# Kernel optimization log

Measured on AMD Instinct MI355X. Metric: run time of the kernel, lower is better.

Reference implementation:

```python
import jax, jax.numpy as jnp
import numpy as np

N_NODES = 100000
N_EDGES = 1600000
IN_CH, HID_CH, OUT_CH = 128, 128, 64


def _sage_conv(x, src, dst, Wl, bl, Wr, num_nodes):
    # PyG SAGEConv (aggr='mean', root_weight=True):
    #   out_i = W_l @ mean_{j in N(i)} x_j + b_l + W_r @ x_i
    msgs = x[src]                                            # [E, d] gather
    agg = jax.ops.segment_sum(msgs, dst, num_segments=num_nodes)   # [N, d]
    cnt = jax.ops.segment_sum(jnp.ones((src.shape[0],), x.dtype), dst,
                              num_segments=num_nodes)              # [N]
    mean = agg / jnp.maximum(cnt, 1.0)[:, None]
    return mean @ Wl.T + bl + x @ Wr.T


def setup_inputs() -> dict:
    key = jax.random.key(0)
    ks = jax.random.split(key, 8)
    x = jax.random.normal(ks[0], (N_NODES, IN_CH), dtype=jnp.float32)
    edge_index = jax.random.randint(ks[1], (2, N_EDGES), 0, N_NODES, dtype=jnp.int32)
    s1 = 1.0 / np.sqrt(IN_CH)
    s2 = 1.0 / np.sqrt(HID_CH)
    Wl1 = jax.random.uniform(ks[2], (HID_CH, IN_CH), jnp.float32, -s1, s1)
    bl1 = jax.random.uniform(ks[3], (HID_CH,), jnp.float32, -s1, s1)
    Wr1 = jax.random.uniform(ks[4], (HID_CH, IN_CH), jnp.float32, -s1, s1)
    Wl2 = jax.random.uniform(ks[5], (OUT_CH, HID_CH), jnp.float32, -s2, s2)
    bl2 = jax.random.uniform(ks[6], (OUT_CH,), jnp.float32, -s2, s2)
    Wr2 = jax.random.uniform(ks[7], (OUT_CH, HID_CH), jnp.float32, -s2, s2)
    return {"x": x, "edge_index": edge_index, "Wl1": Wl1, "bl1": bl1,
            "Wr1": Wr1, "Wl2": Wl2, "bl2": bl2, "Wr2": Wr2}


def reference(x, edge_index, Wl1, bl1, Wr1, Wl2, bl2, Wr2):
    src, dst = edge_index[0], edge_index[1]
    n = x.shape[0]
    h = _sage_conv(x, src, dst, Wl1, bl1, Wr1, n)
    h = jax.nn.relu(h)  # dropout is identity in eval mode
    out = _sage_conv(h, src, dst, Wl2, bl2, Wr2, n)
    return out
```

## Files before the change

### kernel.cpp

```cpp
#include <hip/hip_runtime.h>
#include <hip/hip_bf16.h>
#include <stdint.h>

#define IN_CH 128
#define NPB   448
#define NBUCK 224
#define CAP   8192
#define PART_EPB 2048
#define SRC_BITS 17
#define SRC_MASK ((1 << SRC_BITS) - 1)

typedef short v8s __attribute__((ext_vector_type(8)));
typedef float v4f __attribute__((ext_vector_type(4)));
typedef float v2f __attribute__((ext_vector_type(2)));
typedef ushort v4u __attribute__((ext_vector_type(4)));

__device__ __forceinline__ ushort f2b(float f) {
    return ((__hip_bfloat16_raw)__float2bfloat16(f)).x;
}
__device__ __forceinline__ float b2f(ushort u) {
    __hip_bfloat16_raw r; r.x = u;
    return __bfloat162float((__hip_bfloat16)r);
}

#define ACC4(r) {                                                            \
    a01 += (v2f){__uint_as_float((r).x << 16),                               \
                 __uint_as_float((r).x & 0xffff0000u)};                      \
    a23 += (v2f){__uint_as_float((r).y << 16),                               \
                 __uint_as_float((r).y & 0xffff0000u)};                      \
    a45 += (v2f){__uint_as_float((r).z << 16),                               \
                 __uint_as_float((r).z & 0xffff0000u)};                      \
    a67 += (v2f){__uint_as_float((r).w << 16),                               \
                 __uint_as_float((r).w & 0xffff0000u)}; }

__global__ __launch_bounds__(256) void k_part_gemm1(
    const int* __restrict__ src, const int* __restrict__ dst,
    int* __restrict__ cursor, int* __restrict__ ebuf, int E, int PB,
    const float* __restrict__ Af,
    const float* __restrict__ WlF, const float* __restrict__ WrF,
    ushort* __restrict__ qb, ushort* __restrict__ pbb, int N) {
    __shared__ __align__(16) char smem[69632];
    int tid = threadIdx.x;

    if ((int)blockIdx.x < PB) {
        int* sedge = (int*)smem;
        int* sdst  = (int*)(smem + 8192);
        int* h     = (int*)(smem + 16384);
        int* lofs  = h + NBUCK;
        int* gbase = lofs + NBUCK;
        int* lcur  = gbase + NBUCK;
        int* ssc   = lcur + NBUCK;
        unsigned char* sbuck = (unsigned char*)(ssc + 256);

        int eb0 = blockIdx.x * PART_EPB;
        int cnt = min(PART_EPB, E - eb0);

        if (tid < NBUCK) { h[tid] = 0; lcur[tid] = 0; }
        __syncthreads();
        for (int i = tid; i < cnt; i += 256) {
            int d = dst[eb0 + i];
            sdst[i] = d;
            atomicAdd(&h[d / NPB], 1);
        }
        __syncthreads();
        int v = (tid < NBUCK) ? h[tid] : 0;
        ssc[tid] = v;
        __syncthreads();
        for (int off = 1; off < 256; off <<= 1) {
            int val = (tid >= off) ? ssc[tid - off] : 0;
            __syncthreads();
            ssc[tid] += val;
            __syncthreads();
        }
        int excl = ssc[tid] - v;
        if (tid < NBUCK) {
            lofs[tid] = excl;
            gbase[tid] = tid * CAP + atomicAdd(&cursor[tid], v);
        }
        __syncthreads();
        for (int i = tid; i < cnt; i += 256) {
            int s0 = src[eb0 + i];
            int d0 = sdst[i];
            int b = d0 / NPB;
            int dl = d0 - b * NPB;
            int p = atomicAdd(&lcur[b], 1);
            int slot = lofs[b] + p;
            sedge[slot] = (dl << SRC_BITS) | s0;
            sbuck[slot] = (unsigned char)b;
        }
        __syncthreads();
        for (int i = tid; i < cnt; i += 256) {
            int b = sbuck[i];
            int pos = gbase[b] + (i - lofs[b]);
            if (pos < (b + 1) * CAP) ebuf[pos] = sedge[i];
        }
        return;
    }

    const int OC = 256;
    const int NT = OC / 16;
    const int LDW = 128 + 8;
    ushort* Wlds = (ushort*)smem;

    int gb = blockIdx.x - PB;
    if (gb == 0 && tid < 16) {
        v8s z = {0, 0, 0, 0, 0, 0, 0, 0};
        *(v8s*)(qb + (size_t)N * 128 + tid * 8) = z;
    }

    for (int it = 0; it < OC / 16; it++) {
        int idx = it * 256 + tid;
        int r = idx >> 4, kc = (idx & 15) * 8;
        const float* Wrow = (r < OC / 2) ? (WlF + (size_t)r * 128)
                                         : (WrF + (size_t)(r - OC / 2) * 128);
        float4 w0 = *(const float4*)(Wrow + kc);
        float4 w1 = *(const float4*)(Wrow + kc + 4);
        v8s wv;
        wv[0] = (short)f2b(w0.x); wv[1] = (short)f2b(w0.y);
        wv[2] = (short)f2b(w0.z); wv[3] = (short)f2b(w0.w);
        wv[4] = (short)f2b(w1.x); wv[5] = (short)f2b(w1.y);
        wv[6] = (short)f2b(w1.z); wv[7] = (short)f2b(w1.w);
        *(v8s*)((short*)Wlds + r * LDW + kc) = wv;
    }
    __syncthreads();

    int wave = tid >> 6;
    int lane = tid & 63;
    int m16 = lane & 15;
    int quad = lane >> 4;
    int rowbase = gb * 128 + wave * 32;

    v4f acc[2][NT];
#pragma unroll
    for (int mt = 0; mt < 2; mt++)
#pragma unroll
        for (int t = 0; t < NT; t++) acc[mt][t] = {0.f, 0.f, 0.f, 0.f};

    int ar0 = min(rowbase + m16, N - 1);
    int ar1 = min(rowbase + 16 + m16, N - 1);

#pragma unroll
    for (int ks = 0; ks < 4; ks++) {
        int k0 = ks * 32 + quad * 8;
        float4 f00 = *(const float4*)(Af + (size_t)ar0 * 128 + k0);
        float4 f01 = *(const float4*)(Af + (size_t)ar0 * 128 + k0 + 4);
        float4 f10 = *(const float4*)(Af + (size_t)ar1 * 128 + k0);
        float4 f11 = *(const float4*)(Af + (size_t)ar1 * 128 + k0 + 4);
        v8s a0, a1;
        a0[0] = (short)f2b(f00.x); a0[1] = (short)f2b(f00.y);
        a0[2] = (short)f2b(f00.z); a0[3] = (short)f2b(f00.w);
        a0[4] = (short)f2b(f01.x); a0[5] = (short)f2b(f01.y);
        a0[6] = (short)f2b(f01.z); a0[7] = (short)f2b(f01.w);
        a1[0] = (short)f2b(f10.x); a1[1] = (short)f2b(f10.y);
        a1[2] = (short)f2b(f10.z); a1[3] = (short)f2b(f10.w);
        a1[4] = (short)f2b(f11.x); a1[5] = (short)f2b(f11.y);
        a1[6] = (short)f2b(f11.z); a1[7] = (short)f2b(f11.w);
#pragma unroll
        for (int t = 0; t < NT; t++) {
            v8s b = *(const v8s*)((const short*)Wlds + (t * 16 + m16) * LDW + k0);
            acc[0][t] = __builtin_amdgcn_mfma_f32_16x16x32_bf16(a0, b, acc[0][t], 0, 0, 0);
            acc[1][t] = __builtin_amdgcn_mfma_f32_16x16x32_bf16(a1, b, acc[1][t], 0, 0, 0);
        }
    }

#pragma unroll
    for (int mt = 0; mt < 2; mt++) {
        int orow0 = rowbase + mt * 16 + quad * 4;
#pragma unroll
        for (int r = 0; r < 4; r++) {
            int orow = orow0 + r;
            if (orow < N) {
#pragma unroll
                for (int t = 0; t < NT; t++) {
                    int c = t * 16 + m16;
                    float v = acc[mt][t][r];
                    if (c < 128) qb[(size_t)orow * 128 + c] = f2b(v);
                    else pbb[(size_t)orow * 128 + (c - 128)] = f2b(v);
                }
            }
        }
    }
}

__global__ __launch_bounds__(256) void k_bbuild(
    const int* __restrict__ ebuf, const int* __restrict__ cursor,
    int2* __restrict__ rowdeg, int* __restrict__ col, int N) {
    __shared__ int sdeg[NPB];
    __shared__ int scur[NPB];
    __shared__ int ssum[256];
    int b = blockIdx.x, tid = threadIdx.x;
    int base = b * NPB;
    int nodes = min(NPB, N - base);
    int e0 = b * CAP;
    int e1 = e0 + min(cursor[b], CAP);

    for (int i = tid; i < NPB; i += 256) sdeg[i] = 0;
    __syncthreads();
    for (int e = e0 + tid; e < e1; e += 256)
        atomicAdd(&sdeg[((unsigned)ebuf[e]) >> SRC_BITS], 1);
    __syncthreads();
    int d0 = 0, d1 = 0;
    if (tid < 224) { d0 = sdeg[2 * tid]; d1 = sdeg[2 * tid + 1]; }
    int ts = d0 + d1;
    ssum[tid] = ts;
    __syncthreads();
    for (int off = 1; off < 256; off <<= 1) {
        int val = (tid >= off) ? ssum[tid - off] : 0;
        __syncthreads();
        ssum[tid] += val;
        __syncthreads();
    }
    int excl = ssum[tid] - ts;
    if (tid < 224) {
        scur[2 * tid] = excl;
        scur[2 * tid + 1] = excl + d0;
        if (2 * tid < nodes)
            rowdeg[base + 2 * tid] = make_int2(e0 + excl, d0);
        if (2 * tid + 1 < nodes)
            rowdeg[base + 2 * tid + 1] = make_int2(e0 + excl + d0, d1);
    }
    __syncthreads();
    for (int e = e0 + tid; e < e1; e += 256) {
        int w = ebuf[e];
        int dl = ((unsigned)w) >> SRC_BITS;
        int p = atomicAdd(&scur[dl], 1);
        col[e0 + p] = w & SRC_MASK;
    }
}

__global__ __launch_bounds__(256) void k_wgemm2(
    const ushort* __restrict__ Ab,
    const float* __restrict__ WlF, const float* __restrict__ WrF,
    ushort* __restrict__ qb, float* __restrict__ pbf, int N) {
    const int OC = 128;
    const int NT = OC / 16;
    const int LDW = 128 + 8;
    __shared__ ushort Wlds[OC * LDW];

    int tid = threadIdx.x;
    if (blockIdx.x == 0 && tid < 8) {
        v8s z = {0, 0, 0, 0, 0, 0, 0, 0};
        *(v8s*)(qb + (size_t)N * 64 + tid * 8) = z;
    }
    for (int it = 0; it < OC / 16; it++) {
        int idx = it * 256 + tid;
        int r = idx >> 4, kc = (idx & 15) * 8;
        const float* Wrow = (r < OC / 2) ? (WlF + (size_t)r * 128)
                                         : (WrF + (size_t)(r - OC / 2) * 128);
        float4 w0 = *(const float4*)(Wrow + kc);
        float4 w1 = *(const float4*)(Wrow + kc + 4);
        v8s wv;
        wv[0] = (short)f2b(w0.x); wv[1] = (short)f2b(w0.y);
        wv[2] = (short)f2b(w0.z); wv[3] = (short)f2b(w0.w);
        wv[4] = (short)f2b(w1.x); wv[5] = (short)f2b(w1.y);
        wv[6] = (short)f2b(w1.z); wv[7] = (short)f2b(w1.w);
        *(v8s*)((short*)Wlds + r * LDW + kc) = wv;
    }
    __syncthreads();

    int wave = tid >> 6;
    int lane = tid & 63;
    int m16 = lane & 15;
    int quad = lane >> 4;
    int rowbase = blockIdx.x * 128 + wave * 32;

    v4f acc[2][NT];
#pragma unroll
    for (int mt = 0; mt < 2; mt++)
#pragma unroll
        for (int t = 0; t < NT; t++) acc[mt][t] = {0.f, 0.f, 0.f, 0.f};

    int ar0 = min(rowbase + m16, N - 1);
    int ar1 = min(rowbase + 16 + m16, N - 1);

#pragma unroll
    for (int ks = 0; ks < 4; ks++) {
        int k0 = ks * 32 + quad * 8;
        v8s a0 = *(const v8s*)((const short*)Ab + (size_t)ar0 * 128 + k0);
        v8s a1 = *(const v8s*)((const short*)Ab + (size_t)ar1 * 128 + k0);
#pragma unroll
        for (int t = 0; t < NT; t++) {
            v8s b = *(const v8s*)((const short*)Wlds + (t * 16 + m16) * LDW + k0);
            acc[0][t] = __builtin_amdgcn_mfma_f32_16x16x32_bf16(a0, b, acc[0][t], 0, 0, 0);
            acc[1][t] = __builtin_amdgcn_mfma_f32_16x16x32_bf16(a1, b, acc[1][t], 0, 0, 0);
        }
    }

#pragma unroll
    for (int mt = 0; mt < 2; mt++) {
        int orow0 = rowbase + mt * 16 + quad * 4;
#pragma unroll
        for (int r = 0; r < 4; r++) {
            int orow = orow0 + r;
            if (orow < N) {
#pragma unroll
                for (int t = 0; t < NT; t++) {
                    int c = t * 16 + m16;
                    float v = acc[mt][t][r];
                    if (c < 64) qb[(size_t)orow * 64 + c] = f2b(v);
                    else pbf[(size_t)orow * 64 + (c - 64)] = v;
                }
            }
        }
    }
}

__global__ __launch_bounds__(256, 8) void k_agg1(
    const int2* __restrict__ rowdeg,
    const int* __restrict__ col, const ushort* __restrict__ q1b,
    const ushort* __restrict__ p1b, const float* __restrict__ bias,
    ushort* __restrict__ hb, int N) {
    int node = blockIdx.x * (blockDim.x >> 6) + (threadIdx.x >> 6);
    int lane = threadIdx.x & 63;
    if (node >= N) return;
    int2 rd = rowdeg[node];
    int s0 = rd.x, dn = rd.y;
    int s1 = s0 + dn;
    int g = lane >> 4;
    int ch = 8 * (lane & 15);
    v4u pb = *(const v4u*)((const ushort*)p1b + (size_t)node * 128 + ch);
    v4u pb2 = *(const v4u*)((const ushort*)p1b + (size_t)node * 128 + ch + 4);
    int last = (dn > 0) ? (s1 - 1) : s0;
    v2f a01 = {0.f, 0.f}, a23 = {0.f, 0.f}, a45 = {0.f, 0.f}, a67 = {0.f, 0.f};
    int j = s0;
    do {
        int i0 = j + g,      i1 = j + 4 + g,  i2 = j + 8 + g,  i3 = j + 12 + g;
        int i4 = j + 16 + g, i5 = j + 20 + g, i6 = j + 24 + g, i7 = j + 28 + g;
        int t0 = col[min(i0, last)];
        int t1 = col[min(i1, last)];
        int t2 = col[min(i2, last)];
        int t3 = col[min(i3, last)];
        int t4 = col[min(i4, last)];
        int t5 = col[min(i5, last)];
        int t6 = col[min(i6, last)];
        int t7 = col[min(i7, last)];
        int c0 = (i0 < s1) ? t0 : N;
        int c1 = (i1 < s1) ? t1 : N;
        int c2 = (i2 < s1) ? t2 : N;
        int c3 = (i3 < s1) ? t3 : N;
        int c4 = (i4 < s1) ? t4 : N;
        int c5 = (i5 < s1) ? t5 : N;
        int c6 = (i6 < s1) ? t6 : N;
        int c7 = (i7 < s1) ? t7 : N;
        uint4 r0 = *(const uint4*)(q1b + ((uint)c0 * 128u + (uint)ch));
        uint4 r1 = *(const uint4*)(q1b + ((uint)c1 * 128u + (uint)ch));
        uint4 r2 = *(const uint4*)(q1b + ((uint)c2 * 128u + (uint)ch));
        uint4 r3 = *(const uint4*)(q1b + ((uint)c3 * 128u + (uint)ch));
        uint4 r4 = *(const uint4*)(q1b + ((uint)c4 * 128u + (uint)ch));
        uint4 r5 = *(const uint4*)(q1b + ((uint)c5 * 128u + (uint)ch));
        uint4 r6 = *(const uint4*)(q1b + ((uint)c6 * 128u + (uint)ch));
        uint4 r7 = *(const uint4*)(q1b + ((uint)c7 * 128u + (uint)ch));
        ACC4(r0); ACC4(r1); ACC4(r2); ACC4(r3);
        ACC4(r4); ACC4(r5); ACC4(r6); ACC4(r7);
        j += 32;
    } while (j < s1);
    float s[8] = {a01.x, a01.y, a23.x, a23.y, a45.x, a45.y, a67.x, a67.y};
#pragma unroll
    for (int k = 0; k < 8; k++) {
        s[k] += __shfl_xor(s[k], 16);
        s[k] += __shfl_xor(s[k], 32);
    }
    if (g == 0) {
        float inv = (dn > 0) ? 1.0f / (float)dn : 0.0f;
        float4 bi0 = *(const float4*)(bias + ch);
        float4 bi1 = *(const float4*)(bias + ch + 4);
        v8s o;
        o[0] = (short)f2b(fmaxf(s[0] * inv + b2f(pb.x) + bi0.x, 0.f));
        o[1] = (short)f2b(fmaxf(s[1] * inv + b2f(pb.y) + bi0.y, 0.f));
        o[2] = (short)f2b(fmaxf(s[2] * inv + b2f(pb.z) + bi0.z, 0.f));
        o[3] = (short)f2b(fmaxf(s[3] * inv + b2f(pb.w) + bi0.w, 0.f));
        o[4] = (short)f2b(fmaxf(s[4] * inv + b2f(pb2.x) + bi1.x, 0.f));
        o[5] = (short)f2b(fmaxf(s[5] * inv + b2f(pb2.y) + bi1.y, 0.f));
        o[6] = (short)f2b(fmaxf(s[6] * inv + b2f(pb2.z) + bi1.z, 0.f));
        o[7] = (short)f2b(fmaxf(s[7] * inv + b2f(pb2.w) + bi1.w, 0.f));
        *(v8s*)(hb + (size_t)node * 128 + ch) = o;
    }
}

__global__ __launch_bounds__(256, 8) void k_agg2(
    const int2* __restrict__ rowdeg,
    const int* __restrict__ col, const ushort* __restrict__ q2,
    const float* __restrict__ p2, const float* __restrict__ bias,
    float* __restrict__ out, int N) {
    int node = blockIdx.x * (blockDim.x >> 6) + (threadIdx.x >> 6);
    int lane = threadIdx.x & 63;
    if (node >= N) return;
    int2 rd = rowdeg[node];
    int s0 = rd.x, dn = rd.y;
    int s1 = s0 + dn;
    int g = lane >> 3;
    int ch = 8 * (lane & 7);
    v4f p0 = *(const v4f*)(p2 + (size_t)node * 64 + ch);
    v4f p1 = *(const v4f*)(p2 + (size_t)node * 64 + ch + 4);
    int last = (dn > 0) ? (s1 - 1) : s0;
    v2f a01 = {0.f, 0.f}, a23 = {0.f, 0.f}, a45 = {0.f, 0.f}, a67 = {0.f, 0.f};
    int j = s0;
    do {
        int i0 = j + g, i1 = j + 8 + g, i2 = j + 16 + g, i3 = j + 24 + g;
        int t0 = col[min(i0, last)];
        int t1 = col[min(i1, last)];
        int t2 = col[min(i2, last)];
        int t3 = col[min(i3, last)];
        int c0 = (i0 < s1) ? t0 : N;
        int c1 = (i1 < s1) ? t1 : N;
        int c2 = (i2 < s1) ? t2 : N;
        int c3 = (i3 < s1) ? t3 : N;
        uint4 r0 = *(const uint4*)(q2 + ((uint)c0 * 64u + (uint)ch));
        uint4 r1 = *(const uint4*)(q2 + ((uint)c1 * 64u + (uint)ch));
        uint4 r2 = *(const uint4*)(q2 + ((uint)c2 * 64u + (uint)ch));
        uint4 r3 = *(const uint4*)(q2 + ((uint)c3 * 64u + (uint)ch));
        ACC4(r0); ACC4(r1); ACC4(r2); ACC4(r3);
        j += 32;
    } while (j < s1);
    float s[8] = {a01.x, a01.y, a23.x, a23.y, a45.x, a45.y, a67.x, a67.y};
#pragma unroll
    for (int k = 0; k < 8; k++) {
        s[k] += __shfl_xor(s[k], 8);
        s[k] += __shfl_xor(s[k], 16);
        s[k] += __shfl_xor(s[k], 32);
    }
    if (g == 0) {
        float inv = (dn > 0) ? 1.0f / (float)dn : 0.0f;
        float4 bi0 = *(const float4*)(bias + ch);
        float4 bi1 = *(const float4*)(bias + ch + 4);
        v4f o0, o1;
        o0[0] = s[0] * inv + p0[0] + bi0.x;
        o0[1] = s[1] * inv + p0[1] + bi0.y;
        o0[2] = s[2] * inv + p0[2] + bi0.z;
        o0[3] = s[3] * inv + p0[3] + bi0.w;
        o1[0] = s[4] * inv + p1[0] + bi1.x;
        o1[1] = s[5] * inv + p1[1] + bi1.y;
        o1[2] = s[6] * inv + p1[2] + bi1.z;
        o1[3] = s[7] * inv + p1[3] + bi1.w;
        *(v4f*)(out + (size_t)node * 64 + ch) = o0;
        *(v4f*)(out + (size_t)node * 64 + ch + 4) = o1;
    }
}

extern "C" void kernel_launch(void* const* d_in, const int* in_sizes, int n_in,
                              void* d_out, int out_size, void* d_ws, size_t ws_size,
                              hipStream_t stream) {
    const float* x   = (const float*)d_in[0];
    const int* ei    = (const int*)d_in[1];
    const float* Wl1 = (const float*)d_in[2];
    const float* bl1 = (const float*)d_in[3];
    const float* Wr1 = (const float*)d_in[4];
    const float* Wl2 = (const float*)d_in[5];
    const float* bl2 = (const float*)d_in[6];
    const float* Wr2 = (const float*)d_in[7];

    const int N = in_sizes[0] / IN_CH;
    const int E = in_sizes[1] / 2;
    const int* src = ei;
    const int* dst = ei + E;

    char* p = (char*)d_ws;
    auto carve = [&](size_t bytes) -> void* {
        void* q = (void*)p;
        p += (bytes + 255) & ~(size_t)255;
        return q;
    };
    int* cursor   = (int*)carve(NBUCK * 4);
    int* ebuf     = (int*)carve((size_t)NBUCK * CAP * 4);
    int* col      = (int*)carve((size_t)NBUCK * CAP * 4 + 256);
    int2* rowdeg  = (int2*)carve((size_t)N * 8);
    ushort* q1b   = (ushort*)carve(((size_t)N + 1) * 128 * 2);
    ushort* p1b   = (ushort*)carve((size_t)N * 128 * 2);
    ushort* hb    = (ushort*)carve((size_t)N * 128 * 2);
    ushort* q2    = (ushort*)carve(((size_t)N + 1) * 64 * 2);
    float* p2     = (float*)carve((size_t)N * 64 * 4);
    (void)ws_size; (void)n_in;

    float* out = (float*)d_out;
    (void)out_size;

    const int PB  = (E + PART_EPB - 1) / PART_EPB;
    const int GB  = (N + 127) / 128;

    (void)hipMemsetAsync(cursor, 0, NBUCK * 4, stream);
    k_part_gemm1<<<PB + GB, 256, 0, stream>>>(
        src, dst, cursor, ebuf, E, PB, x, Wl1, Wr1, q1b, p1b, N);

    k_bbuild<<<NBUCK, 256, 0, stream>>>(ebuf, cursor, rowdeg, col, N);

    k_agg1<<<(N + 3) / 4, 256, 0, stream>>>(rowdeg, col, q1b, p1b, bl1, hb, N);

    k_wgemm2<<<GB, 256, 0, stream>>>(hb, Wl2, Wr2, q2, p2, N);
    k_agg2<<<(N + 3) / 4, 256, 0, stream>>>(rowdeg, col, q2, p2, bl2, out, N);
}
```

Before: 284.3 us.

## Pair bucket CSR build with layer-1 GEMM instead of edge partitioning

The edge partitioning pass becomes its own small kernel. The per-bucket CSR build is merged with the layer-1 dense GEMM into one launch, so the 224 bbuild blocks run alongside the GEMM blocks rather than as a separate serial launch. Partition blocks no longer carry the GEMM's large shared-memory footprint, and the sbuck array grows from bytes to ints. The risk is that bbuild blocks now hold the GEMM-sized shared memory allocation, which can lower their occupancy.

```diff
diff --git a/kernel.cpp b/kernel.cpp
--- a/kernel.cpp
+++ b/kernel.cpp
@@ -33,76 +33,119 @@
     a67 += (v2f){__uint_as_float((r).w << 16),                               \
                  __uint_as_float((r).w & 0xffff0000u)}; }
 
-__global__ __launch_bounds__(256) void k_part_gemm1(
+__global__ __launch_bounds__(256) void k_part(
     const int* __restrict__ src, const int* __restrict__ dst,
-    int* __restrict__ cursor, int* __restrict__ ebuf, int E, int PB,
+    int* __restrict__ cursor, int* __restrict__ ebuf, int E) {
+    __shared__ int sedge[PART_EPB];
+    __shared__ int sdst[PART_EPB];
+    __shared__ int sbuck[PART_EPB];
+    __shared__ int h[NBUCK], lofs[NBUCK], gbase[NBUCK], lcur[NBUCK];
+    __shared__ int ssc[256];
+
+    int tid = threadIdx.x;
+    int eb0 = blockIdx.x * PART_EPB;
+    int cnt = min(PART_EPB, E - eb0);
+
+    if (tid < NBUCK) { h[tid] = 0; lcur[tid] = 0; }
+    __syncthreads();
+    for (int i = tid; i < cnt; i += 256) {
+        int d = dst[eb0 + i];
+        sdst[i] = d;
+        atomicAdd(&h[d / NPB], 1);
+    }
+    __syncthreads();
+    int v = (tid < NBUCK) ? h[tid] : 0;
+    ssc[tid] = v;
+    __syncthreads();
+    for (int off = 1; off < 256; off <<= 1) {
+        int val = (tid >= off) ? ssc[tid - off] : 0;
+        __syncthreads();
+        ssc[tid] += val;
+        __syncthreads();
+    }
+    int excl = ssc[tid] - v;
+    if (tid < NBUCK) {
+        lofs[tid] = excl;
+        gbase[tid] = tid * CAP + atomicAdd(&cursor[tid], v);
+    }
+    __syncthreads();
+    for (int i = tid; i < cnt; i += 256) {
+        int s0 = src[eb0 + i];
+        int d0 = sdst[i];
+        int b = d0 / NPB;
+        int dl = d0 - b * NPB;
+        int p = atomicAdd(&lcur[b], 1);
+        int slot = lofs[b] + p;
+        sedge[slot] = (dl << SRC_BITS) | s0;
+        sbuck[slot] = b;
+    }
+    __syncthreads();
+    for (int i = tid; i < cnt; i += 256) {
+        int b = sbuck[i];
+        int pos = gbase[b] + (i - lofs[b]);
+        if (pos < (b + 1) * CAP) ebuf[pos] = sedge[i];
+    }
+}
+
+__global__ __launch_bounds__(256) void k_bbuild_gemm1(
+    const int* __restrict__ ebuf, const int* __restrict__ cursor,
+    int2* __restrict__ rowdeg, int* __restrict__ col,
     const float* __restrict__ Af,
     const float* __restrict__ WlF, const float* __restrict__ WrF,
     ushort* __restrict__ qb, ushort* __restrict__ pbb, int N) {
-    __shared__ __align__(16) char smem[69632];
-    int tid = threadIdx.x;
-
-    if ((int)blockIdx.x < PB) {
-        int* sedge = (int*)smem;
-        int* sdst  = (int*)(smem + 8192);
-        int* h     = (int*)(smem + 16384);
-        int* lofs  = h + NBUCK;
-        int* gbase = lofs + NBUCK;
-        int* lcur  = gbase + NBUCK;
-        int* ssc   = lcur + NBUCK;
-        unsigned char* sbuck = (unsigned char*)(ssc + 256);
-
-        int eb0 = blockIdx.x * PART_EPB;
-        int cnt = min(PART_EPB, E - eb0);
-
-        if (tid < NBUCK) { h[tid] = 0; lcur[tid] = 0; }
-        __syncthreads();
-        for (int i = tid; i < cnt; i += 256) {
-            int d = dst[eb0 + i];
-            sdst[i] = d;
-            atomicAdd(&h[d / NPB], 1);
-        }
-        __syncthreads();
-        int v = (tid < NBUCK) ? h[tid] : 0;
-        ssc[tid] = v;
-        __syncthreads();
-        for (int off = 1; off < 256; off <<= 1) {
-            int val = (tid >= off) ? ssc[tid - off] : 0;
-            __syncthreads();
-            ssc[tid] += val;
-            __syncthreads();
-        }
-        int excl = ssc[tid] - v;
-        if (tid < NBUCK) {
-            lofs[tid] = excl;
-            gbase[tid] = tid * CAP + atomicAdd(&cursor[tid], v);
-        }
-        __syncthreads();
-        for (int i = tid; i < cnt; i += 256) {
-            int s0 = src[eb0 + i];
-            int d0 = sdst[i];
-            int b = d0 / NPB;
-            int dl = d0 - b * NPB;
-            int p = atomicAdd(&lcur[b], 1);
-            int slot = lofs[b] + p;
-            sedge[slot] = (dl << SRC_BITS) | s0;
-            sbuck[slot] = (unsigned char)b;
-        }
-        __syncthreads();
-        for (int i = tid; i < cnt; i += 256) {
-            int b = sbuck[i];
-            int pos = gbase[b] + (i - lofs[b]);
-            if (pos < (b + 1) * CAP) ebuf[pos] = sedge[i];
-        }
-        return;
-    }
-
     const int OC = 256;
     const int NT = OC / 16;
     const int LDW = 128 + 8;
-    ushort* Wlds = (ushort*)smem;
-
-    int gb = blockIdx.x - PB;
+    __shared__ ushort Wlds[OC * LDW];
+    __shared__ int sdeg[NPB];
+    __shared__ int scur[NPB];
+    __shared__ int ssum[256];
+
+    int tid = threadIdx.x;
+
+    if (blockIdx.x < NBUCK) {
+        int b = blockIdx.x;
+        int base = b * NPB;
+        int nodes = min(NPB, N - base);
+        int e0 = b * CAP;
+        int e1 = e0 + min(cursor[b], CAP);
+
+        for (int i = tid; i < NPB; i += 256) sdeg[i] = 0;
+        __syncthreads();
+        for (int e = e0 + tid; e < e1; e += 256)
+            atomicAdd(&sdeg[((unsigned)ebuf[e]) >> SRC_BITS], 1);
+        __syncthreads();
+        int d0 = 0, d1 = 0;
+        if (tid < 224) { d0 = sdeg[2 * tid]; d1 = sdeg[2 * tid + 1]; }
+        int ts = d0 + d1;
+        ssum[tid] = ts;
+        __syncthreads();
+        for (int off = 1; off < 256; off <<= 1) {
+            int val = (tid >= off) ? ssum[tid - off] : 0;
+            __syncthreads();
+            ssum[tid] += val;
+            __syncthreads();
+        }
+        int excl = ssum[tid] - ts;
+        if (tid < 224) {
+            scur[2 * tid] = excl;
+            scur[2 * tid + 1] = excl + d0;
+            if (2 * tid < nodes)
+                rowdeg[base + 2 * tid] = make_int2(e0 + excl, d0);
+            if (2 * tid + 1 < nodes)
+                rowdeg[base + 2 * tid + 1] = make_int2(e0 + excl + d0, d1);
+        }
+        __syncthreads();
+        for (int e = e0 + tid; e < e1; e += 256) {
+            int w = ebuf[e];
+            int dl = ((unsigned)w) >> SRC_BITS;
+            int p = atomicAdd(&scur[dl], 1);
+            col[e0 + p] = w & SRC_MASK;
+        }
+        return;
+    }
+
+    int gb = blockIdx.x - NBUCK;
     if (gb == 0 && tid < 16) {
         v8s z = {0, 0, 0, 0, 0, 0, 0, 0};
         *(v8s*)(qb + (size_t)N * 128 + tid * 8) = z;
@@ -179,52 +222,6 @@
                 }
             }
         }
-    }
-}
-
-__global__ __launch_bounds__(256) void k_bbuild(
-    const int* __restrict__ ebuf, const int* __restrict__ cursor,
-    int2* __restrict__ rowdeg, int* __restrict__ col, int N) {
-    __shared__ int sdeg[NPB];
-    __shared__ int scur[NPB];
-    __shared__ int ssum[256];
-    int b = blockIdx.x, tid = threadIdx.x;
-    int base = b * NPB;
-    int nodes = min(NPB, N - base);
-    int e0 = b * CAP;
-    int e1 = e0 + min(cursor[b], CAP);
-
-    for (int i = tid; i < NPB; i += 256) sdeg[i] = 0;
-    __syncthreads();
-    for (int e = e0 + tid; e < e1; e += 256)
-        atomicAdd(&sdeg[((unsigned)ebuf[e]) >> SRC_BITS], 1);
-    __syncthreads();
-    int d0 = 0, d1 = 0;
-    if (tid < 224) { d0 = sdeg[2 * tid]; d1 = sdeg[2 * tid + 1]; }
-    int ts = d0 + d1;
-    ssum[tid] = ts;
-    __syncthreads();
-    for (int off = 1; off < 256; off <<= 1) {
-        int val = (tid >= off) ? ssum[tid - off] : 0;
-        __syncthreads();
-        ssum[tid] += val;
-        __syncthreads();
-    }
-    int excl = ssum[tid] - ts;
-    if (tid < 224) {
-        scur[2 * tid] = excl;
-        scur[2 * tid + 1] = excl + d0;
-        if (2 * tid < nodes)
-            rowdeg[base + 2 * tid] = make_int2(e0 + excl, d0);
-        if (2 * tid + 1 < nodes)
-            rowdeg[base + 2 * tid + 1] = make_int2(e0 + excl + d0, d1);
-    }
-    __syncthreads();
-    for (int e = e0 + tid; e < e1; e += 256) {
-        int w = ebuf[e];
-        int dl = ((unsigned)w) >> SRC_BITS;
-        int p = atomicAdd(&scur[dl], 1);
-        col[e0 + p] = w & SRC_MASK;
     }
 }
 
@@ -474,14 +471,13 @@
     float* out = (float*)d_out;
     (void)out_size;
 
-    const int PB  = (E + PART_EPB - 1) / PART_EPB;
-    const int GB  = (N + 127) / 128;
+    const int PB = (E + PART_EPB - 1) / PART_EPB;
+    const int GB = (N + 127) / 128;
 
     (void)hipMemsetAsync(cursor, 0, NBUCK * 4, stream);
-    k_part_gemm1<<<PB + GB, 256, 0, stream>>>(
-        src, dst, cursor, ebuf, E, PB, x, Wl1, Wr1, q1b, p1b, N);
-
-    k_bbuild<<<NBUCK, 256, 0, stream>>>(ebuf, cursor, rowdeg, col, N);
+    k_part<<<PB, 256, 0, stream>>>(src, dst, cursor, ebuf, E);
+    k_bbuild_gemm1<<<NBUCK + GB, 256, 0, stream>>>(
+        ebuf, cursor, rowdeg, col, x, Wl1, Wr1, q1b, p1b, N);
 
     k_agg1<<<(N + 3) / 4, 256, 0, stream>>>(rowdeg, col, q1b, p1b, bl1, hb, N);
 
```

Measured after the change: 279.2 us. About the same (-1.8%).
